# Kernel optimization log

Measured on AMD Instinct MI355X. Metric: run time of the kernel, lower is better.

## Reference

```python
import jax, jax.numpy as jnp
import numpy as np

TOKENS, IN_DIM, VOCAB = 2048, 2048, 32000
TILE_FACTOR = 16


def setup_inputs() -> dict:
    key = jax.random.key(0)
    k1, k2, k3 = jax.random.split(key, 3)
    inp = jax.random.normal(k1, (TOKENS, IN_DIM), dtype=jnp.float32)
    target = jax.random.randint(k2, (TOKENS,), 0, VOCAB, dtype=jnp.int64)
    # LM-head weight, shape [out_dim(vocab), in_dim] as in nn.Linear
    proj_weight = jax.random.normal(k3, (VOCAB, IN_DIM), dtype=jnp.float32) * 0.02
    return {"input": inp, "target": target, "proj_weight": proj_weight}


def reference(input, target, proj_weight):
    # Original loops over token tiles: for each tile, logits = tile @ W.T,
    # then softmax over vocab (dim=-1). Softmax is per-row (per-token), so the
    # concatenation of per-tile outputs equals the full row-wise softmax.
    # target is accepted but unused, matching the original forward.
    logits = jnp.einsum('td,vd->tv', input, proj_weight)  # [tokens, vocab]
    return jax.nn.softmax(logits, axis=-1)
```

## Files before the change

### kernel.cpp

```cpp
#include <hip/hip_runtime.h>
#include <hip/hip_bf16.h>
#include <math.h>

#define TOKENS 2048
#define IN_DIM 2048
#define VOCAB  32000

#define BM 256
#define BN 256
#define BK 64
#define NKSTEP (IN_DIM / BK)
#define GEMM_GRID ((TOKENS / BM) * (VOCAB / BN))

typedef short s16x8 __attribute__((ext_vector_type(8)));
typedef float f32x4 __attribute__((ext_vector_type(4)));

__device__ __forceinline__ unsigned short f2bf_rne(float f) {
  unsigned int u = __float_as_uint(f);
  u += 0x7fffu + ((u >> 16) & 1u);
  return (unsigned short)(u >> 16);
}

__global__ __launch_bounds__(256) void convert_f32_to_bf16(
    const float* __restrict__ in, unsigned short* __restrict__ out, int n4) {
  int idx = blockIdx.x * blockDim.x + threadIdx.x;
  int stride = gridDim.x * blockDim.x;
  for (int i = idx; i < n4; i += stride) {
    float4 v = reinterpret_cast<const float4*>(in)[i];
    ushort4 o;
    o.x = f2bf_rne(v.x);
    o.y = f2bf_rne(v.y);
    o.z = f2bf_rne(v.z);
    o.w = f2bf_rne(v.w);
    reinterpret_cast<ushort4*>(out)[i] = o;
  }
}

__device__ __forceinline__ void gload_lds16(const unsigned short* g, unsigned short* l) {
  __builtin_amdgcn_global_load_lds(
      (const __attribute__((address_space(1))) unsigned int*)g,
      (__attribute__((address_space(3))) unsigned int*)l, 16, 0, 0);
}

__global__ __launch_bounds__(512, 2) void gemm_bt(
    const unsigned short* __restrict__ A,
    const unsigned short* __restrict__ B,
    float* __restrict__ C) {
  __shared__ __align__(16) unsigned short lds[65536];

  const int tid = threadIdx.x;
  const int lane = tid & 63;
  const int wave = tid >> 6;
  const int wr = wave >> 2;
  const int wc = wave & 3;

  const int bid = blockIdx.x;
  const int lid = (bid & 7) * (GEMM_GRID / 8) + (bid >> 3);
  const int rowTile = lid & 7;
  const int colTile = lid >> 3;
  const int rowBase = rowTile * BM;
  const int colBase = colTile * BN;

  const int r0 = tid >> 3;
  const int r1 = 64 + r0;
  const int c8 = (((tid & 7) ^ (r0 & 7)) << 3);
  const unsigned short* srcA0 = A + (size_t)(rowBase + r0) * IN_DIM + c8;
  const unsigned short* srcA1 = A + (size_t)(rowBase + r1) * IN_DIM + c8;
  const unsigned short* srcB0 = B + (size_t)(colBase + r0) * IN_DIM + c8;
  const unsigned short* srcB1 = B + (size_t)(colBase + r1) * IN_DIM + c8;
  const int ldsD0 = tid * 8;
  const int ldsD1 = (512 + tid) * 8;

  auto stageA = [&](int buf, int h, int k) {
    size_t off = (size_t)h * (128 * IN_DIM) + k;
    int dst = buf * 32768 + h * 8192;
    gload_lds16(srcA0 + off, &lds[dst + ldsD0]);
    gload_lds16(srcA1 + off, &lds[dst + ldsD1]);
  };
  auto stageB = [&](int buf, int h, int k) {
    size_t off = (size_t)h * (128 * IN_DIM) + k;
    int dst = 16384 + buf * 32768 + h * 8192;
    gload_lds16(srcB0 + off, &lds[dst + ldsD0]);
    gload_lds16(srcB1 + off, &lds[dst + ldsD1]);
  };

  const int sc0 = (((lane >> 4) ^ (lane & 7)) << 3);
  const int sc1 = (((4 + (lane >> 4)) ^ (lane & 7)) << 3);
  const int aRow = (wr * 128 + (lane & 15)) * 64;
  const int bRow = 16384 + (wc * 64 + (lane & 15)) * 64;

#define LDA(buf, m, kk) (*(const s16x8*)&lds[(buf) * 32768 + aRow + (m) * 1024 + ((kk) ? sc1 : sc0)])
#define LDB(buf, n, kk) (*(const s16x8*)&lds[(buf) * 32768 + bRow + (n) * 1024 + ((kk) ? sc1 : sc0)])

  f32x4 acc[8][4] = {};

  stageA(0, 0, 0);
  stageA(0, 1, 0);
  stageB(0, 0, 0);
  stageB(0, 1, 0);
  stageA(1, 0, 64);
  asm volatile("s_waitcnt vmcnt(2)" ::: "memory");
  __builtin_amdgcn_s_barrier();

#define KSTEP(bufc, kc, kn1, kn2)                                                   \
  {                                                                                 \
    s16x8 aL[4][2], aH[4][2], bL[2][2], bH[2][2];                                   \
                   \
    _Pragma("unroll") for (int m = 0; m < 4; ++m) {                                 \
      aL[m][0] = LDA(bufc, m, 0);                                                   \
      aL[m][1] = LDA(bufc, m, 1);                                                   \
    }                                                                               \
    _Pragma("unroll") for (int n = 0; n < 2; ++n) {                                 \
      bL[n][0] = LDB(bufc, n, 0);                                                   \
      bL[n][1] = LDB(bufc, n, 1);                                                   \
    }                                                                               \
    stageA((bufc) ^ 1, 1, kn1);                                                     \
    asm volatile("s_waitcnt lgkmcnt(8)" ::: "memory");                              \
    __builtin_amdgcn_s_barrier();                                                   \
    asm volatile("s_waitcnt lgkmcnt(0)" ::: "memory");                              \
    __builtin_amdgcn_s_setprio(1);                                                  \
    _Pragma("unroll") for (int m = 0; m < 4; ++m)                                   \
        _Pragma("unroll") for (int n = 0; n < 2; ++n) {                             \
      acc[m][n] = __builtin_amdgcn_mfma_f32_16x16x32_bf16(aL[m][0], bL[n][0], acc[m][n], 0, 0, 0); \
      acc[m][n] = __builtin_amdgcn_mfma_f32_16x16x32_bf16(aL[m][1], bL[n][1], acc[m][n], 0, 0, 0); \
    }                                                                               \
    __builtin_amdgcn_s_setprio(0);                                                  \
    __builtin_amdgcn_s_barrier();                                                   \
                                   \
    _Pragma("unroll") for (int m = 0; m < 4; ++m) {                                 \
      aH[m][0] = LDA(bufc, 4 + m, 0);                                               \
      aH[m][1] = LDA(bufc, 4 + m, 1);                                               \
    }                                                                               \
    stageB((bufc) ^ 1, 0, kn1);                                                     \
    __builtin_amdgcn_s_barrier();                                                   \
    asm volatile("s_waitcnt lgkmcnt(0)" ::: "memory");                              \
    __builtin_amdgcn_s_setprio(1);                                                  \
    _Pragma("unroll") for (int m = 0; m < 4; ++m)                                   \
        _Pragma("unroll") for (int n = 0; n < 2; ++n) {                             \
      acc[4 + m][n] = __builtin_amdgcn_mfma_f32_16x16x32_bf16(aH[m][0], bL[n][0], acc[4 + m][n], 0, 0, 0); \
      acc[4 + m][n] = __builtin_amdgcn_mfma_f32_16x16x32_bf16(aH[m][1], bL[n][1], acc[4 + m][n], 0, 0, 0); \
    }                                                                               \
    __builtin_amdgcn_s_setprio(0);                                                  \
    __builtin_amdgcn_s_barrier();                                                   \
                                   \
    _Pragma("unroll") for (int n = 0; n < 2; ++n) {                                 \
      bH[n][0] = LDB(bufc, 2 + n, 0);                                               \
      bH[n][1] = LDB(bufc, 2 + n, 1);                                               \
    }                                                                               \
    stageB((bufc) ^ 1, 1, kn1);                                                     \
    __builtin_amdgcn_s_barrier();                                                   \
    asm volatile("s_waitcnt lgkmcnt(0)" ::: "memory");                              \
    __builtin_amdgcn_s_setprio(1);                                                  \
    _Pragma("unroll") for (int m = 0; m < 4; ++m)                                   \
        _Pragma("unroll") for (int n = 0; n < 2; ++n) {                             \
      acc[4 + m][2 + n] = __builtin_amdgcn_mfma_f32_16x16x32_bf16(aH[m][0], bH[n][0], acc[4 + m][2 + n], 0, 0, 0); \
      acc[4 + m][2 + n] = __builtin_amdgcn_mfma_f32_16x16x32_bf16(aH[m][1], bH[n][1], acc[4 + m][2 + n], 0, 0, 0); \
    }                                                                               \
    __builtin_amdgcn_s_setprio(0);                                                  \
    __builtin_amdgcn_s_barrier();                                                   \
     \
     \
    stageA((bufc), 0, kn2);                                                         \
    asm volatile("s_waitcnt vmcnt(2)" ::: "memory");                                \
    __builtin_amdgcn_s_barrier();                                                   \
    __builtin_amdgcn_s_setprio(1);                                                  \
    _Pragma("unroll") for (int m = 0; m < 4; ++m)                                   \
        _Pragma("unroll") for (int n = 0; n < 2; ++n) {                             \
      acc[m][2 + n] = __builtin_amdgcn_mfma_f32_16x16x32_bf16(aL[m][0], bH[n][0], acc[m][2 + n], 0, 0, 0); \
      acc[m][2 + n] = __builtin_amdgcn_mfma_f32_16x16x32_bf16(aL[m][1], bH[n][1], acc[m][2 + n], 0, 0, 0); \
    }                                                                               \
    __builtin_amdgcn_s_setprio(0);                                                  \
    __builtin_amdgcn_s_barrier();                                                   \
  }

  for (int i = 0; i < NKSTEP / 2; ++i) {
    const int k = i * 128;
    KSTEP(0, k, (k + 64) & (IN_DIM - 1), (k + 128) & (IN_DIM - 1));
    KSTEP(1, k + 64, (k + 128) & (IN_DIM - 1), (k + 192) & (IN_DIM - 1));
  }

  asm volatile("s_waitcnt vmcnt(0)" ::: "memory");

#pragma unroll
  for (int m = 0; m < 8; ++m) {
    int row0 = rowBase + wr * 128 + m * 16 + ((lane >> 4) << 2);
#pragma unroll
    for (int n = 0; n < 4; ++n) {
      int col = colBase + wc * 64 + n * 16 + (lane & 15);
#pragma unroll
      for (int j = 0; j < 4; ++j) {
        C[(size_t)(row0 + j) * VOCAB + col] = acc[m][n][j];
      }
    }
  }
#undef LDA
#undef LDB
#undef KSTEP
}

__global__ __launch_bounds__(256) void row_softmax(float* __restrict__ C) {
  const int row = blockIdx.x;
  float* p = C + (size_t)row * VOCAB;
  const int tid = threadIdx.x;
  const int NQ = VOCAB / 4;

  float m = -3.4e38f, s = 0.f;
  for (int i = tid; i < NQ; i += 256) {
    float4 v = reinterpret_cast<const float4*>(p)[i];
    float mv = fmaxf(fmaxf(v.x, v.y), fmaxf(v.z, v.w));
    if (mv > m) {
      s *= __expf(m - mv);
      m = mv;
    }
    s += __expf(v.x - m) + __expf(v.y - m) + __expf(v.z - m) + __expf(v.w - m);
  }
#pragma unroll
  for (int off = 32; off > 0; off >>= 1) {
    float m2 = __shfl_down(m, off);
    float s2 = __shfl_down(s, off);
    float M = fmaxf(m, m2);
    s = s * __expf(m - M) + s2 * __expf(m2 - M);
    m = M;
  }
  __shared__ float redM[4], redS[4];
  if ((tid & 63) == 0) {
    redM[tid >> 6] = m;
    redS[tid >> 6] = s;
  }
  __syncthreads();
  if (tid == 0) {
    float M = redM[0], S = redS[0];
#pragma unroll
    for (int w = 1; w < 4; ++w) {
      float M2 = fmaxf(M, redM[w]);
      S = S * __expf(M - M2) + redS[w] * __expf(redM[w] - M2);
      M = M2;
    }
    redM[0] = M;
    redS[0] = 1.f / S;
  }
  __syncthreads();
  const float M = redM[0], invS = redS[0];
  for (int i = tid; i < NQ; i += 256) {
    float4 v = reinterpret_cast<const float4*>(p)[i];
    v.x = __expf(v.x - M) * invS;
    v.y = __expf(v.y - M) * invS;
    v.z = __expf(v.z - M) * invS;
    v.w = __expf(v.w - M) * invS;
    reinterpret_cast<float4*>(p)[i] = v;
  }
}

extern "C" void kernel_launch(void* const* d_in, const int* in_sizes, int n_in,
                              void* d_out, int out_size, void* d_ws, size_t ws_size,
                              hipStream_t stream) {
  const float* x = (const float*)d_in[0];
  const float* w = (const float*)d_in[2];
  float* out = (float*)d_out;

  unsigned short* xbf = (unsigned short*)d_ws;
  unsigned short* wbf = xbf + (size_t)TOKENS * IN_DIM;

  convert_f32_to_bf16<<<512, 256, 0, stream>>>(x, xbf, TOKENS * IN_DIM / 4);
  convert_f32_to_bf16<<<2048, 256, 0, stream>>>(w, wbf, VOCAB * IN_DIM / 4);
  gemm_bt<<<GEMM_GRID, 512, 0, stream>>>(xbf, wbf, out);
  row_softmax<<<TOKENS, 256, 0, stream>>>(out);
}
```

Before: 526.4 us.

## Fuse per-tile softmax max/sum into GEMM epilogue and deepen load prefetch

The GEMM epilogue now computes a per-row max and exp-sum for each 256-column tile and writes them to a partials buffer. A small kernel merges these into a per-row max and inverse sum, and the softmax pass becomes a single read-modify-write over the logits instead of two full reads. The stage-load schedule is also reordered so more global loads are in flight (the vmcnt threshold moves from 2 to 6). In exchange the GEMM epilogue gains shuffle reductions and an LDS round-trip, and it adds an extra launch plus workspace for the partials.

```diff
diff --git a/kernel.cpp b/kernel.cpp
--- a/kernel.cpp
+++ b/kernel.cpp
@@ -11,6 +11,7 @@
 #define BK 64
 #define NKSTEP (IN_DIM / BK)
 #define GEMM_GRID ((TOKENS / BM) * (VOCAB / BN))
+#define NCT (VOCAB / BN)
 
 typedef short s16x8 __attribute__((ext_vector_type(8)));
 typedef float f32x4 __attribute__((ext_vector_type(4)));
@@ -45,7 +46,8 @@
 __global__ __launch_bounds__(512, 2) void gemm_bt(
     const unsigned short* __restrict__ A,
     const unsigned short* __restrict__ B,
-    float* __restrict__ C) {
+    float* __restrict__ C,
+    float2* __restrict__ partials) {
   __shared__ __align__(16) unsigned short lds[65536];
 
   const int tid = threadIdx.x;
@@ -99,13 +101,15 @@
   stageB(0, 0, 0);
   stageB(0, 1, 0);
   stageA(1, 0, 64);
-  asm volatile("s_waitcnt vmcnt(2)" ::: "memory");
+  stageA(1, 1, 64);
+  stageB(1, 0, 64);
+  asm volatile("s_waitcnt vmcnt(6)" ::: "memory");
   __builtin_amdgcn_s_barrier();
 
-#define KSTEP(bufc, kc, kn1, kn2)                                                   \
+#define KSTEP(bufc, kn1, kn2)                                                       \
   {                                                                                 \
     s16x8 aL[4][2], aH[4][2], bL[2][2], bH[2][2];                                   \
-                   \
+                                   \
     _Pragma("unroll") for (int m = 0; m < 4; ++m) {                                 \
       aL[m][0] = LDA(bufc, m, 0);                                                   \
       aL[m][1] = LDA(bufc, m, 1);                                                   \
@@ -114,7 +118,7 @@
       bL[n][0] = LDB(bufc, n, 0);                                                   \
       bL[n][1] = LDB(bufc, n, 1);                                                   \
     }                                                                               \
-    stageA((bufc) ^ 1, 1, kn1);                                                     \
+    stageB((bufc) ^ 1, 1, kn1);                                                     \
     asm volatile("s_waitcnt lgkmcnt(8)" ::: "memory");                              \
     __builtin_amdgcn_s_barrier();                                                   \
     asm volatile("s_waitcnt lgkmcnt(0)" ::: "memory");                              \
@@ -126,12 +130,11 @@
     }                                                                               \
     __builtin_amdgcn_s_setprio(0);                                                  \
     __builtin_amdgcn_s_barrier();                                                   \
-                                   \
+                                                      \
     _Pragma("unroll") for (int m = 0; m < 4; ++m) {                                 \
       aH[m][0] = LDA(bufc, 4 + m, 0);                                               \
       aH[m][1] = LDA(bufc, 4 + m, 1);                                               \
     }                                                                               \
-    stageB((bufc) ^ 1, 0, kn1);                                                     \
     __builtin_amdgcn_s_barrier();                                                   \
     asm volatile("s_waitcnt lgkmcnt(0)" ::: "memory");                              \
     __builtin_amdgcn_s_setprio(1);                                                  \
@@ -142,12 +145,13 @@
     }                                                                               \
     __builtin_amdgcn_s_setprio(0);                                                  \
     __builtin_amdgcn_s_barrier();                                                   \
-                                   \
+     \
     _Pragma("unroll") for (int n = 0; n < 2; ++n) {                                 \
       bH[n][0] = LDB(bufc, 2 + n, 0);                                               \
       bH[n][1] = LDB(bufc, 2 + n, 1);                                               \
     }                                                                               \
-    stageB((bufc) ^ 1, 1, kn1);                                                     \
+    stageA((bufc), 0, kn2);                                                         \
+    stageA((bufc), 1, kn2);                                                         \
     __builtin_amdgcn_s_barrier();                                                   \
     asm volatile("s_waitcnt lgkmcnt(0)" ::: "memory");                              \
     __builtin_amdgcn_s_setprio(1);                                                  \
@@ -158,11 +162,9 @@
     }                                                                               \
     __builtin_amdgcn_s_setprio(0);                                                  \
     __builtin_amdgcn_s_barrier();                                                   \
-     \
-     \
-    stageA((bufc), 0, kn2);                                                         \
-    asm volatile("s_waitcnt vmcnt(2)" ::: "memory");                                \
-    __builtin_amdgcn_s_barrier();                                                   \
+          \
+         \
+    stageB((bufc), 0, kn2);                                                         \
     __builtin_amdgcn_s_setprio(1);                                                  \
     _Pragma("unroll") for (int m = 0; m < 4; ++m)                                   \
         _Pragma("unroll") for (int n = 0; n < 2; ++n) {                             \
@@ -170,16 +172,18 @@
       acc[m][2 + n] = __builtin_amdgcn_mfma_f32_16x16x32_bf16(aL[m][1], bH[n][1], acc[m][2 + n], 0, 0, 0); \
     }                                                                               \
     __builtin_amdgcn_s_setprio(0);                                                  \
+    asm volatile("s_waitcnt vmcnt(6)" ::: "memory");                                \
     __builtin_amdgcn_s_barrier();                                                   \
   }
 
   for (int i = 0; i < NKSTEP / 2; ++i) {
     const int k = i * 128;
-    KSTEP(0, k, (k + 64) & (IN_DIM - 1), (k + 128) & (IN_DIM - 1));
-    KSTEP(1, k + 64, (k + 128) & (IN_DIM - 1), (k + 192) & (IN_DIM - 1));
+    KSTEP(0, (k + 64) & (IN_DIM - 1), (k + 128) & (IN_DIM - 1));
+    KSTEP(1, (k + 128) & (IN_DIM - 1), (k + 192) & (IN_DIM - 1));
   }
 
   asm volatile("s_waitcnt vmcnt(0)" ::: "memory");
+  __syncthreads();
 
 #pragma unroll
   for (int m = 0; m < 8; ++m) {
@@ -193,55 +197,66 @@
       }
     }
   }
+
+  float* lmax = reinterpret_cast<float*>(lds);
+  float* lsum = lmax + 1024;
+#pragma unroll
+  for (int m = 0; m < 8; ++m) {
+#pragma unroll
+    for (int jj = 0; jj < 4; ++jj) {
+      float v0 = acc[m][0][jj], v1 = acc[m][1][jj], v2 = acc[m][2][jj], v3 = acc[m][3][jj];
+      float mx = fmaxf(fmaxf(v0, v1), fmaxf(v2, v3));
+#pragma unroll
+      for (int off = 1; off < 16; off <<= 1) mx = fmaxf(mx, __shfl_xor(mx, off));
+      float s = __expf(v0 - mx) + __expf(v1 - mx) + __expf(v2 - mx) + __expf(v3 - mx);
+#pragma unroll
+      for (int off = 1; off < 16; off <<= 1) s += __shfl_xor(s, off);
+      if ((lane & 15) == 0) {
+        int r = wr * 128 + m * 16 + ((lane >> 4) << 2) + jj;
+        lmax[r * 4 + wc] = mx;
+        lsum[r * 4 + wc] = s;
+      }
+    }
+  }
+  __syncthreads();
+  if (tid < 256) {
+    float m0 = lmax[tid * 4 + 0], m1 = lmax[tid * 4 + 1];
+    float m2 = lmax[tid * 4 + 2], m3 = lmax[tid * 4 + 3];
+    float M = fmaxf(fmaxf(m0, m1), fmaxf(m2, m3));
+    float S = lsum[tid * 4 + 0] * __expf(m0 - M) + lsum[tid * 4 + 1] * __expf(m1 - M) +
+              lsum[tid * 4 + 2] * __expf(m2 - M) + lsum[tid * 4 + 3] * __expf(m3 - M);
+    partials[(size_t)(rowBase + tid) * NCT + colTile] = make_float2(M, S);
+  }
 #undef LDA
 #undef LDB
 #undef KSTEP
 }
 
-__global__ __launch_bounds__(256) void row_softmax(float* __restrict__ C) {
+__global__ __launch_bounds__(256) void reduce_stats(
+    const float2* __restrict__ partials, float2* __restrict__ stats) {
+  int row = blockIdx.x * blockDim.x + threadIdx.x;
+  if (row >= TOKENS) return;
+  const float2* p = partials + (size_t)row * NCT;
+  float M = -3.4e38f, S = 0.f;
+  for (int i = 0; i < NCT; ++i) {
+    float2 v = p[i];
+    if (v.x > M) {
+      S *= __expf(M - v.x);
+      M = v.x;
+    }
+    S += v.y * __expf(v.x - M);
+  }
+  stats[row] = make_float2(M, 1.f / S);
+}
+
+__global__ __launch_bounds__(256) void apply_softmax(
+    float* __restrict__ C, const float2* __restrict__ stats) {
   const int row = blockIdx.x;
   float* p = C + (size_t)row * VOCAB;
-  const int tid = threadIdx.x;
+  const float2 st = stats[row];
+  const float M = st.x, invS = st.y;
   const int NQ = VOCAB / 4;
-
-  float m = -3.4e38f, s = 0.f;
-  for (int i = tid; i < NQ; i += 256) {
-    float4 v = reinterpret_cast<const float4*>(p)[i];
-    float mv = fmaxf(fmaxf(v.x, v.y), fmaxf(v.z, v.w));
-    if (mv > m) {
-      s *= __expf(m - mv);
-      m = mv;
-    }
-    s += __expf(v.x - m) + __expf(v.y - m) + __expf(v.z - m) + __expf(v.w - m);
-  }
-#pragma unroll
-  for (int off = 32; off > 0; off >>= 1) {
-    float m2 = __shfl_down(m, off);
-    float s2 = __shfl_down(s, off);
-    float M = fmaxf(m, m2);
-    s = s * __expf(m - M) + s2 * __expf(m2 - M);
-    m = M;
-  }
-  __shared__ float redM[4], redS[4];
-  if ((tid & 63) == 0) {
-    redM[tid >> 6] = m;
-    redS[tid >> 6] = s;
-  }
-  __syncthreads();
-  if (tid == 0) {
-    float M = redM[0], S = redS[0];
-#pragma unroll
-    for (int w = 1; w < 4; ++w) {
-      float M2 = fmaxf(M, redM[w]);
-      S = S * __expf(M - M2) + redS[w] * __expf(redM[w] - M2);
-      M = M2;
-    }
-    redM[0] = M;
-    redS[0] = 1.f / S;
-  }
-  __syncthreads();
-  const float M = redM[0], invS = redS[0];
-  for (int i = tid; i < NQ; i += 256) {
+  for (int i = threadIdx.x; i < NQ; i += 256) {
     float4 v = reinterpret_cast<const float4*>(p)[i];
     v.x = __expf(v.x - M) * invS;
     v.y = __expf(v.y - M) * invS;
@@ -260,9 +275,12 @@
 
   unsigned short* xbf = (unsigned short*)d_ws;
   unsigned short* wbf = xbf + (size_t)TOKENS * IN_DIM;
+  float2* partials = (float2*)(wbf + (size_t)VOCAB * IN_DIM);
+  float2* stats = partials + (size_t)TOKENS * NCT;
 
   convert_f32_to_bf16<<<512, 256, 0, stream>>>(x, xbf, TOKENS * IN_DIM / 4);
   convert_f32_to_bf16<<<2048, 256, 0, stream>>>(w, wbf, VOCAB * IN_DIM / 4);
-  gemm_bt<<<GEMM_GRID, 512, 0, stream>>>(xbf, wbf, out);
-  row_softmax<<<TOKENS, 256, 0, stream>>>(out);
-}
+  gemm_bt<<<GEMM_GRID, 512, 0, stream>>>(xbf, wbf, out, partials);
+  reduce_stats<<<TOKENS / 256, 256, 0, stream>>>(partials, stats);
+  apply_softmax<<<TOKENS, 256, 0, stream>>>(out, stats);
+}
```

Result: faster. 485.9 us (-7.7%).
